# Optimization experiments

Measured on AMD Instinct MI355X. Metric: run time of the kernel, lower is better.

Reference implementation:

```python
import jax, jax.numpy as jnp
import numpy as np

B, IN_DIM, N, L = 8, 2, 512, 64
D_MODEL = 32
D_FF = 32          # must equal D_MODEL: output_bn is BatchNorm2d(d_model) applied to skip
DEPTH = 3          # blocks=3 * layers=1; dilation resets to 1 each block -> all dilations = 1
KS = 2             # temporal kernel size
EPS = 1e-5         # BatchNorm eps


def setup_inputs() -> dict:
    key = jax.random.key(0)
    ks = jax.random.split(key, 16)
    s = 0.1  # weight scale for numeric sanity
    x = jax.random.normal(ks[0], (B, IN_DIM, N, L), jnp.float32)
    a = jax.random.uniform(ks[1], (N, N), jnp.float32)
    adj = a / a.sum(axis=1, keepdims=True)  # row-stochastic diffusion matrix
    return {
        "x": x,
        "adj": adj,
        "Wstart": jax.random.normal(ks[2], (D_MODEL, IN_DIM), jnp.float32) * s,
        "bstart": jnp.zeros((D_MODEL,), jnp.float32),
        "Wf": jax.random.normal(ks[3], (DEPTH, D_MODEL, D_MODEL, KS), jnp.float32) * s,
        "bf": jnp.zeros((DEPTH, D_MODEL), jnp.float32),
        "Wg": jax.random.normal(ks[4], (DEPTH, D_MODEL, D_MODEL, KS), jnp.float32) * s,
        "bg": jnp.zeros((DEPTH, D_MODEL), jnp.float32),
        "Wskip": jax.random.normal(ks[5], (DEPTH, D_FF, D_MODEL), jnp.float32) * s,
        "bskip": jnp.zeros((DEPTH, D_FF), jnp.float32),
        "Wgc": jax.random.normal(ks[6], (DEPTH, D_MODEL, 3 * D_MODEL), jnp.float32) * s,
        "bgc": jnp.zeros((DEPTH, D_MODEL), jnp.float32),
        "gcbn_g": jnp.ones((DEPTH, D_MODEL), jnp.float32),
        "gcbn_b": jnp.zeros((DEPTH, D_MODEL), jnp.float32),
        "bn_g": jnp.ones((DEPTH, D_MODEL), jnp.float32),
        "bn_b": jnp.zeros((DEPTH, D_MODEL), jnp.float32),
        "obn_g": jnp.ones((D_MODEL,), jnp.float32),
        "obn_b": jnp.zeros((D_MODEL,), jnp.float32),
    }


def _c1x1(x, W, b):
    # Conv2d with (1,1) kernel == channel mixing. x: [b,c,n,l], W: [o,c]
    return jnp.einsum('bcnl,oc->bonl', x, W) + b[None, :, None, None]


def _dconv(x, W, b, d):
    # Conv2d kernel (1,2), dilation d along time (valid). W: [o,c,2]
    Lx = x.shape[-1]
    y = (jnp.einsum('bcnl,oc->bonl', x[..., :Lx - d], W[..., 0])
         + jnp.einsum('bcnl,oc->bonl', x[..., d:], W[..., 1]))
    return y + b[None, :, None, None]


def _bn(x, g, bta):
    # eval-mode BatchNorm2d: running_mean=0, running_var=1
    inv = g / jnp.sqrt(1.0 + EPS)
    return x * inv[None, :, None, None] + bta[None, :, None, None]


def reference(x, adj, Wstart, bstart, Wf, bf, Wg, bg, Wskip, bskip,
              Wgc, bgc, gcbn_g, gcbn_b, bn_g, bn_b, obn_g, obn_b):
    rf = 1 + DEPTH * (KS - 1)  # receptive field with dilation 1 per layer
    h = _c1x1(x, Wstart, bstart)
    if h.shape[-1] < rf:
        h = jnp.pad(h, ((0, 0), (0, 0), (0, 0), (rf - h.shape[-1], 0)))
    skip = None
    for i in range(DEPTH):
        residual = h
        filt = jnp.tanh(_dconv(h, Wf[i], bf[i], 1))
        gate = jax.nn.sigmoid(_dconv(h, Wg[i], bg[i], 1))
        h = filt * gate
        s = _c1x1(h, Wskip[i], bskip[i])
        skip = s if skip is None else s + skip[..., -s.shape[-1]:]
        if i == DEPTH - 1:
            break
        # order-2 graph diffusion: h, A h, A^2 h -> concat -> 1x1 conv -> BN (dropout: eval noop)
        x1 = jnp.einsum('bcnl,nm->bcml', h, adj)
        x2 = jnp.einsum('bcnl,nm->bcml', x1, adj)
        cat = jnp.concatenate([h, x1, x2], axis=1)
        g = _bn(_c1x1(cat, Wgc[i], bgc[i]), gcbn_g[i], gcbn_b[i])
        h = g + residual[..., -g.shape[-1]:]
        h = _bn(h, bn_g[i], bn_b[i])
    out = _bn(skip, obn_g, obn_b)
    return jnp.swapaxes(out, 1, 3)  # [B, L', N, C]
```

## Files before the change

### kernel.cpp

```cpp
#include <hip/hip_runtime.h>
#include <hip/hip_bf16.h>

#define B_     8
#define CIN_   2
#define N_     512
#define C_     32
#define L_     64
#define LOUT_  61
#define BUF_   ((size_t)(8*32*512*64))

typedef __hip_bfloat16 bf16;
typedef unsigned short ushort_t;
typedef unsigned int u32;
typedef __attribute__((ext_vector_type(8))) unsigned short us8;
typedef __attribute__((ext_vector_type(8))) short bf16x8;
typedef __attribute__((ext_vector_type(4))) float f32x4;

static __device__ __forceinline__ float bits2f(ushort_t u) {
    return __uint_as_float(((unsigned)u) << 16);
}
static __device__ __forceinline__ ushort_t f2bits(float v) {
    unsigned u = __float_as_uint(v);
    return (ushort_t)((u + 0x7fffu + ((u >> 16) & 1u)) >> 16);
}

static __device__ __forceinline__ void gload16(const ushort_t* g, ushort_t* l) {
    __builtin_amdgcn_global_load_lds(
        (const __attribute__((address_space(1))) unsigned int*)g,
        (__attribute__((address_space(3))) unsigned int*)l,
        16, 0, 0);
}

static __device__ __forceinline__ u32 swap1(u32 v) {
    return (u32)__builtin_amdgcn_update_dpp(0, (int)v, 0xB1, 0xF, 0xF, true);
}

__global__ void k_start(const float* __restrict__ x,
                        const float* __restrict__ Wst,
                        const float* __restrict__ bst,
                        ushort_t* __restrict__ h) {
    int idx = blockIdx.x * 256 + threadIdx.x;
    int l0 = (idx & 7) * 8;
    int n  = (idx >> 3) & 511;
    int o  = (idx >> 12) & 31;
    int b  = idx >> 17;
    float w0 = Wst[o * 2], w1 = Wst[o * 2 + 1], bb = bst[o];
    int xbase = (b * CIN_ * N_ + n) * L_ + l0;
    float va[8], vb[8];
    *(float4*)&va[0] = *(const float4*)(x + xbase);
    *(float4*)&va[4] = *(const float4*)(x + xbase + 4);
    *(float4*)&vb[0] = *(const float4*)(x + xbase + N_ * L_);
    *(float4*)&vb[4] = *(const float4*)(x + xbase + N_ * L_ + 4);
    us8 r;
    #pragma unroll
    for (int k = 0; k < 8; ++k) r[k] = f2bits(bb + va[k] * w0 + vb[k] * w1);
    *(us8*)(h + (size_t)idx * 8) = r;
}

__global__ void k_transA(const float* __restrict__ adj, ushort_t* __restrict__ adjT) {
    __shared__ float buf[64][65];
    int ti = blockIdx.x & 7;
    int tj = blockIdx.x >> 3;
    int t = threadIdx.x;
    for (int r = 0; r < 16; ++r) {
        int e = t + 256 * r;
        int rl = e >> 6, cl = e & 63;
        buf[rl][cl] = adj[(size_t)(ti * 64 + rl) * 512 + tj * 64 + cl];
    }
    __syncthreads();
    for (int r = 0; r < 16; ++r) {
        int e = t + 256 * r;
        int ml = e >> 6, nl = e & 63;
        adjT[(size_t)(tj * 64 + ml) * 512 + ti * 64 + nl] = f2bits(buf[nl][ml]);
    }
}

__global__ __launch_bounds__(256, 2) void k_sq(const ushort_t* __restrict__ adjT,
                                               ushort_t* __restrict__ adj2T) {
    __shared__ __align__(16) ushort_t lds2[8192];
    ushort_t* As = lds2;
    ushort_t* Bs = lds2 + 4096;
    int mt = blockIdx.x & 7, nc = blockIdx.x >> 3;
    int t = threadIdx.x, lane = t & 63, w = t >> 6;
    int la = lane & 15, q = lane >> 4;
    f32x4 acc[4];
    #pragma unroll
    for (int mi = 0; mi < 4; ++mi) acc[mi] = (f32x4)0.f;
    for (int p0 = 0; p0 < 512; p0 += 64) {
        __syncthreads();
        #pragma unroll
        for (int r = 0; r < 2; ++r) {
            int e = t + 256 * r, ml = e >> 3, oct = e & 7;
            int sw = ((oct + (ml >> 3)) & 7) << 3;
            *(us8*)(As + ml * 64 + sw) =
                *(const us8*)(adjT + (size_t)(mt * 64 + ml) * 512 + p0 + oct * 8);
            *(us8*)(Bs + ml * 64 + sw) =
                *(const us8*)(adjT + (size_t)(p0 + ml) * 512 + nc * 64 + oct * 8);
        }
        __syncthreads();
        #pragma unroll
        for (int ks = 0; ks < 2; ++ks) {
            bf16x8 a[4];
            #pragma unroll
            for (int mi = 0; mi < 4; ++mi) {
                int m = mi * 16 + la;
                int bl = (ks * 4 + q + (m >> 3)) & 7;
                a[mi] = *(const bf16x8*)(As + m * 64 + bl * 8);
            }
            bf16x8 bv;
            {
                int n = w * 16 + la;
                int rot = ((n >> 3) + ks * 4 + q) & 7;
                int col = rot * 8 + (n & 7);
                const ushort_t* p = Bs + (ks * 32 + q * 8) * 64 + col;
                #pragma unroll
                for (int j = 0; j < 8; ++j) bv[j] = (short)p[j * 64];
            }
            #pragma unroll
            for (int mi = 0; mi < 4; ++mi)
                acc[mi] = __builtin_amdgcn_mfma_f32_16x16x32_bf16(a[mi], bv, acc[mi], 0, 0, 0);
        }
    }
    __syncthreads();
    ushort_t* Ys = lds2;
    #pragma unroll
    for (int mi = 0; mi < 4; ++mi)
        #pragma unroll
        for (int r = 0; r < 4; ++r)
            Ys[(mi * 16 + q * 4 + r) * 72 + w * 16 + la] = f2bits(acc[mi][r]);
    __syncthreads();
    #pragma unroll
    for (int r = 0; r < 2; ++r) {
        int e = t + 256 * r, ml = e >> 3, oct = e & 7;
        us8 v = *(const us8*)(Ys + ml * 72 + oct * 8);
        *(us8*)(adj2T + (size_t)(mt * 64 + ml) * 512 + nc * 64 + oct * 8) = v;
    }
}

__global__ __launch_bounds__(256, 4) void k_gs_mfma(
        const ushort_t* __restrict__ h,
        const float* __restrict__ Wf, const float* __restrict__ bfp,
        const float* __restrict__ Wg, const float* __restrict__ bgp,
        const float* __restrict__ Wsk, const float* __restrict__ bsk,
        ushort_t* __restrict__ G, float* __restrict__ out,
        int off, int mode, int storeG,
        const float* __restrict__ og, const float* __restrict__ obb) {
    __shared__ __align__(16) ushort_t lds[9984];
    ushort_t* Hs  = lds;
    ushort_t* Asf = lds + 4096;
    ushort_t* Asg = lds + 6400;
    ushort_t* As2 = lds + 8704;
    __shared__ float bfv[32], bgv[32], bsv[32];
    int t = threadIdx.x;
    int b = blockIdx.x >> 8, n0 = (blockIdx.x & 255) * 2;
    int lane = t & 63, w = t >> 6;
    int ng = w & 1, cg = w >> 1;
    int la = lane & 15, q = lane >> 4;

    const ushort_t* hb = h + (size_t)(b * 32) * 512 * 64;
    #pragma unroll
    for (int r = 0; r < 2; ++r) {
        int e = t + 256 * r;
        int row = e >> 3, s = e & 7;
        int og_ = ((s - row - (row >> 5)) & 7) * 8;
        gload16(hb + ((size_t)(row >> 1) * 512 + n0 + (row & 1)) * 64 + og_,
                Hs + (size_t)e * 8);
    }
    {
        int o = t >> 3, k8 = (t & 7) * 8;
        us8 vf, vg;
        #pragma unroll
        for (int i = 0; i < 8; ++i) {
            int k = k8 + i, c = k & 31, tap = k >> 5;
            vf[i] = f2bits(Wf[o * 64 + c * 2 + tap]);
            vg[i] = f2bits(Wg[o * 64 + c * 2 + tap]);
        }
        *(us8*)(Asf + o * 72 + k8) = vf;
        *(us8*)(Asg + o * 72 + k8) = vg;
        if (k8 < 32) {
            us8 vs;
            #pragma unroll
            for (int i = 0; i < 8; ++i) vs[i] = f2bits(Wsk[o * 32 + k8 + i]);
            *(us8*)(As2 + o * 40 + k8) = vs;
        }
        if (t < 32) { bfv[t] = bfp[t]; bgv[t] = bgp[t]; bsv[t] = bsk[t]; }
    }
    float4 oldv[4];
    #pragma unroll
    for (int i = 0; i < 4; ++i) oldv[i] = make_float4(0.f, 0.f, 0.f, 0.f);
    {
        int col = t >> 1, o0 = (t & 1) * 16;
        int nr = col >> 6, l = col & 63;
        if (mode != 0 && l < LOUT_) {
            const float* po = out + ((size_t)(b * LOUT_ + l) * 512 + n0 + nr) * 32 + o0;
            #pragma unroll
            for (int i = 0; i < 4; ++i) oldv[i] = *(const float4*)(po + i * 4);
        }
    }
    __syncthreads();

    bf16x8 af[2][2], ag[2][2];
    #pragma unroll
    for (int mt = 0; mt < 2; ++mt)
        #pragma unroll
        for (int ks = 0; ks < 2; ++ks) {
            af[mt][ks] = *(const bf16x8*)(Asf + (mt * 16 + la) * 72 + ks * 32 + q * 8);
            ag[mt][ks] = *(const bf16x8*)(Asg + (mt * 16 + la) * 72 + ks * 32 + q * 8);
        }
    bf16x8 a2[2];
    a2[0] = *(const bf16x8*)(As2 + la * 40 + q * 8);
    a2[1] = *(const bf16x8*)(As2 + (16 + la) * 40 + q * 8);

    f32x4 fa[2][2], ga[2][2];
    #pragma unroll
    for (int mt = 0; mt < 2; ++mt)
        #pragma unroll
        for (int cl = 0; cl < 2; ++cl) { fa[mt][cl] = (f32x4)0.f; ga[mt][cl] = (f32x4)0.f; }
    #pragma unroll
    for (int cl = 0; cl < 2; ++cl) {
        int ct = cg * 2 + cl;
        #pragma unroll
        for (int ks = 0; ks < 2; ++ks) {
            int le = ct * 16 + la + ks;
            bf16x8 bv;
            #pragma unroll
            for (int j = 0; j < 8; ++j) {
                int row = (q * 8 + j) * 2 + ng;
                int slot = ((le >> 3) + row + (row >> 5)) & 7;
                bv[j] = (le < 64) ? (short)Hs[row * 64 + (slot & 7) * 8 + (le & 7)] : (short)0;
            }
            #pragma unroll
            for (int mt = 0; mt < 2; ++mt) {
                fa[mt][cl] = __builtin_amdgcn_mfma_f32_16x16x32_bf16(af[mt][ks], bv, fa[mt][cl], 0, 0, 0);
                ga[mt][cl] = __builtin_amdgcn_mfma_f32_16x16x32_bf16(ag[mt][ks], bv, ga[mt][cl], 0, 0, 0);
            }
        }
    }
    __syncthreads();

    #pragma unroll
    for (int mt = 0; mt < 2; ++mt)
        #pragma unroll
        for (int cl = 0; cl < 2; ++cl)
            #pragma unroll
            for (int r = 0; r < 4; ++r) {
                int o = mt * 16 + q * 4 + r;
                float fv = fa[mt][cl][r] + bfv[o];
                float gv = ga[mt][cl][r] + bgv[o];
                float ef = __expf(2.f * fv);
                float act = (1.f - 2.f / (ef + 1.f)) * (1.f / (1.f + __expf(-gv)));
                int l = (cg * 2 + cl) * 16 + la;
                int row = o * 2 + ng;
                int slot = ((l >> 3) + row + (row >> 5)) & 7;
                Hs[row * 64 + slot * 8 + (l & 7)] = f2bits(act);
            }
    __syncthreads();

    if (storeG) {
        #pragma unroll
        for (int r = 0; r < 2; ++r) {
            int e = t + 256 * r;
            int row = e >> 3, s = e & 7;
            int og_ = (s - row - (row >> 5)) & 7;
            us8 v = *(const us8*)(Hs + (size_t)e * 8);
            *(us8*)(G + ((size_t)(b * 32 + (row >> 1)) * 512 + n0 + (row & 1)) * 64 + og_ * 8) = v;
        }
    }
    f32x4 sa[2][2];
    #pragma unroll
    for (int mt = 0; mt < 2; ++mt)
        #pragma unroll
        for (int cl = 0; cl < 2; ++cl) sa[mt][cl] = (f32x4)0.f;
    #pragma unroll
    for (int cl = 0; cl < 2; ++cl) {
        int le = (cg * 2 + cl) * 16 + la + off;
        bf16x8 bv;
        #pragma unroll
        for (int j = 0; j < 8; ++j) {
            int row = (q * 8 + j) * 2 + ng;
            int slot = ((le >> 3) + row + (row >> 5)) & 7;
            bv[j] = (le < 64) ? (short)Hs[row * 64 + (slot & 7) * 8 + (le & 7)] : (short)0;
        }
        sa[0][cl] = __builtin_amdgcn_mfma_f32_16x16x32_bf16(a2[0], bv, sa[0][cl], 0, 0, 0);
        sa[1][cl] = __builtin_amdgcn_mfma_f32_16x16x32_bf16(a2[1], bv, sa[1][cl], 0, 0, 0);
    }
    __syncthreads();

    float* St = (float*)lds;
    const float rbn = rsqrtf(1.f + 1e-5f);
    #pragma unroll
    for (int mt = 0; mt < 2; ++mt)
        #pragma unroll
        for (int cl = 0; cl < 2; ++cl) {
            int col = ng * 64 + (cg * 2 + cl) * 16 + la;
            int ob = mt * 16 + q * 4;
            float4 sv = make_float4(sa[mt][cl][0] + bsv[ob],
                                    sa[mt][cl][1] + bsv[ob + 1],
                                    sa[mt][cl][2] + bsv[ob + 2],
                                    sa[mt][cl][3] + bsv[ob + 3]);
            *(float4*)(St + col * 36 + ob) = sv;
        }
    __syncthreads();
    {
        int col = t >> 1, o0 = (t & 1) * 16;
        int nr = col >> 6, l = col & 63;
        if (l < LOUT_) {
            float* po = out + ((size_t)(b * LOUT_ + l) * 512 + n0 + nr) * 32 + o0;
            #pragma unroll
            for (int i = 0; i < 4; ++i) {
                float4 s = *(float4*)(St + col * 36 + o0 + i * 4);
                if (mode == 0) {
                    *(float4*)(po + i * 4) = s;
                } else {
                    float4 vv = make_float4(oldv[i].x + s.x, oldv[i].y + s.y,
                                            oldv[i].z + s.z, oldv[i].w + s.w);
                    if (mode == 2) {
                        int ob = o0 + i * 4;
                        vv.x = vv.x * (og[ob] * rbn) + obb[ob];
                        vv.y = vv.y * (og[ob + 1] * rbn) + obb[ob + 1];
                        vv.z = vv.z * (og[ob + 2] * rbn) + obb[ob + 2];
                        vv.w = vv.w * (og[ob + 3] * rbn) + obb[ob + 3];
                    }
                    *(float4*)(po + i * 4) = vv;
                }
            }
        }
    }
}

__global__ __launch_bounds__(256, 4) void k_diffuse2(
        const ushort_t* __restrict__ X, const ushort_t* __restrict__ adjT,
        const ushort_t* __restrict__ adj2T,
        ushort_t* __restrict__ Y1, ushort_t* __restrict__ Y2) {
    __shared__ __align__(16) ushort_t lds[16384];
    int cp = blockIdx.x & 15;
    int mt = (blockIdx.x >> 4) & 7;
    int b  = blockIdx.x >> 7;
    int t  = threadIdx.x;
    int lane = t & 63, w = t >> 6;
    int c_loc = w & 1, lh = w >> 1;
    int m0 = mt * 64;
    int la = lane & 15, q = lane >> 4;
    int p_ = la & 1;
    u32 sel = p_ ? 0x07060302u : 0x05040100u;
    const ushort_t* Xb = X + (size_t)(b * 32 + cp * 2) * 512 * 64;
    f32x4 acc1[4][2], acc2[4][2];
    #pragma unroll
    for (int mi = 0; mi < 4; ++mi)
        #pragma unroll
        for (int li = 0; li < 2; ++li) { acc1[mi][li] = (f32x4)0.f; acc2[mi][li] = (f32x4)0.f; }

    union U { u32 u[4]; bf16x8 v; };

    auto STAGE = [&](int n0, ushort_t* bb) {
        ushort_t* As1b = bb;
        ushort_t* As2b = bb + 2048;
        ushort_t* Xsb  = bb + 4096;
        {
            int ml = t >> 2, g = t & 3;
            gload16(adjT  + (size_t)(m0 + ml) * 512 + n0 + g * 8, As1b + (size_t)t * 8);
            gload16(adj2T + (size_t)(m0 + ml) * 512 + n0 + g * 8, As2b + (size_t)t * 8);
        }
        #pragma unroll
        for (int r = 0; r < 2; ++r) {
            int e = t + 256 * r;
            int cl = e >> 8, nl = (e >> 3) & 31, s = e & 7;
            int og = ((s - nl - (nl >> 3)) & 7) * 8;
            gload16(Xb + ((size_t)cl * 512 + n0 + nl) * 64 + og, Xsb + (size_t)e * 8);
        }
    };

    STAGE(0, lds);
    __syncthreads();

    for (int it = 0; it < 16; ++it) {
        ushort_t* cur = lds + (it & 1) * 8192;
        if (it < 15) STAGE((it + 1) * 32, lds + ((it + 1) & 1) * 8192);
        ushort_t* As1 = cur;
        ushort_t* As2 = cur + 2048;
        ushort_t* Xs  = cur + 4096;
        const ushort_t* xc = Xs + c_loc * 2048;
        bf16x8 a1[4], a2v[4];
        #pragma unroll
        for (int mi = 0; mi < 4; ++mi) {
            int m = mi * 16 + la;
            a1[mi]  = *(const bf16x8*)(As1 + m * 32 + q * 8);
            a2v[mi] = *(const bf16x8*)(As2 + m * 32 + q * 8);
        }
        bf16x8 bb[2];
        #pragma unroll
        for (int li = 0; li < 2; ++li) {
            int l2 = lh * 32 + li * 16 + (la & ~1);
            int r0 = q * 8 + p_ * 4;
            int brot = ((l2 >> 3) + p_ * 4 + q) & 7;
            u32 o0 = *(const u32*)(xc + (r0 + 0) * 64 + (((brot + 0) & 7) << 3) + (l2 & 7));
            u32 o1 = *(const u32*)(xc + (r0 + 1) * 64 + (((brot + 1) & 7) << 3) + (l2 & 7));
            u32 o2 = *(const u32*)(xc + (r0 + 2) * 64 + (((brot + 2) & 7) << 3) + (l2 & 7));
            u32 o3 = *(const u32*)(xc + (r0 + 3) * 64 + (((brot + 3) & 7) << 3) + (l2 & 7));
            u32 s0 = swap1(o0), s1 = swap1(o1), s2 = swap1(o2), s3 = swap1(o3);
            u32 lo0 = p_ ? s0 : o0, lo1 = p_ ? s1 : o1;
            u32 lo2 = p_ ? s2 : o2, lo3 = p_ ? s3 : o3;
            u32 hi0 = p_ ? o0 : s0, hi1 = p_ ? o1 : s1;
            u32 hi2 = p_ ? o2 : s2, hi3 = p_ ? o3 : s3;
            U u;
            u.u[0] = __builtin_amdgcn_perm(lo1, lo0, sel);
            u.u[1] = __builtin_amdgcn_perm(lo3, lo2, sel);
            u.u[2] = __builtin_amdgcn_perm(hi1, hi0, sel);
            u.u[3] = __builtin_amdgcn_perm(hi3, hi2, sel);
            bb[li] = u.v;
        }
        #pragma unroll
        for (int mi = 0; mi < 4; ++mi)
            #pragma unroll
            for (int li = 0; li < 2; ++li) {
                acc1[mi][li] = __builtin_amdgcn_mfma_f32_16x16x32_bf16(a1[mi],  bb[li], acc1[mi][li], 0, 0, 0);
                acc2[mi][li] = __builtin_amdgcn_mfma_f32_16x16x32_bf16(a2v[mi], bb[li], acc2[mi][li], 0, 0, 0);
            }
        __syncthreads();
    }

    ushort_t* Ys = lds;
    #pragma unroll
    for (int pass = 0; pass < 2; ++pass) {
        __syncthreads();
        f32x4 (*src)[2] = pass ? acc2 : acc1;
        #pragma unroll
        for (int mi = 0; mi < 4; ++mi)
            #pragma unroll
            for (int li = 0; li < 2; ++li)
                #pragma unroll
                for (int r = 0; r < 4; ++r) {
                    int row = mi * 16 + q * 4 + r;
                    int col = lh * 32 + li * 16 + la;
                    Ys[c_loc * 4608 + row * 72 + col] = f2bits(src[mi][li][r]);
                }
        __syncthreads();
        ushort_t* Yo = pass ? Y2 : Y1;
        int c = t >> 7, mrem = t & 127;
        int m = mrem >> 1, lq = mrem & 1;
        #pragma unroll
        for (int r = 0; r < 4; ++r) {
            int l0 = lq * 32 + r * 8;
            us8 v = *(const us8*)(Ys + c * 4608 + m * 72 + l0);
            *(us8*)(Yo + ((size_t)(b * 32 + cp * 2 + c) * 512 + m0 + m) * 64 + l0) = v;
        }
    }
}

__global__ __launch_bounds__(256, 4) void k_gc3_mfma(
        ushort_t* __restrict__ G, const ushort_t* __restrict__ X1,
        const ushort_t* __restrict__ X2, const ushort_t* __restrict__ hres,
        const float* __restrict__ Wgc, const float* __restrict__ bgc,
        const float* __restrict__ gg, const float* __restrict__ gb,
        const float* __restrict__ bg2, const float* __restrict__ bb2) {
    __shared__ __align__(16) ushort_t cat[192 * 64];
    __shared__ __align__(16) ushort_t hr[64 * 64];
    __shared__ __align__(16) ushort_t Aw[32 * 104];
    __shared__ float prm[5][32];
    int t = threadIdx.x;
    int b = blockIdx.x >> 8, n0 = (blockIdx.x & 255) * 2;
    int lane = t & 63, w = t >> 6;
    int ng = w & 1, cg = w >> 1;
    int la = lane & 15, q = lane >> 4;
    int p_ = la & 1;
    u32 sel = p_ ? 0x07060302u : 0x05040100u;

    #pragma unroll
    for (int r = 0; r < 6; ++r) {
        int e = t + 256 * r;
        int row = e >> 3, s = e & 7;
        int k = row >> 1, nr = row & 1;
        int rot = k + (k >> 3);
        int og = ((s - rot) & 7) * 8;
        const ushort_t* src = (k < 32) ? G : ((k < 64) ? X1 : X2);
        gload16(src + ((size_t)(b * 32 + (k & 31)) * 512 + n0 + nr) * 64 + og,
                cat + (size_t)e * 8);
    }
    #pragma unroll
    for (int r = 0; r < 2; ++r) {
        int e = t + 256 * r;
        int row = e >> 3, oct = e & 7;
        gload16(hres + ((size_t)(b * 32 + (row >> 1)) * 512 + n0 + (row & 1)) * 64 + oct * 8,
                hr + (size_t)e * 8);
    }
    for (int e = t; e < 384; e += 256) {
        int o = e / 12, oct = e % 12;
        us8 v;
        #pragma unroll
        for (int i = 0; i < 8; ++i) v[i] = f2bits(Wgc[o * 96 + oct * 8 + i]);
        *(us8*)(Aw + o * 104 + oct * 8) = v;
    }
    if (t < 32) {
        prm[0][t] = bgc[t]; prm[1][t] = gg[t]; prm[2][t] = gb[t];
        prm[3][t] = bg2[t]; prm[4][t] = bb2[t];
    }
    __syncthreads();

    bf16x8 a[2][3];
    #pragma unroll
    for (int mt = 0; mt < 2; ++mt)
        #pragma unroll
        for (int ks = 0; ks < 3; ++ks)
            a[mt][ks] = *(const bf16x8*)(Aw + (mt * 16 + la) * 104 + ks * 32 + q * 8);

    union U { u32 u[4]; bf16x8 v; };
    f32x4 acc[2][2];
    #pragma unroll
    for (int mt = 0; mt < 2; ++mt)
        #pragma unroll
        for (int cl = 0; cl < 2; ++cl) acc[mt][cl] = (f32x4)0.f;
    #pragma unroll
    for (int cl = 0; cl < 2; ++cl) {
        int l2 = (cg * 2 + cl) * 16 + (la & ~1);
        #pragma unroll
        for (int ks = 0; ks < 3; ++ks) {
            int rb = (ks * 64 + q * 16 + p_ * 8 + ng);
            int brot = ((l2 >> 3) + p_ * 4 + ks * 4 + q) & 7;
            u32 o0 = *(const u32*)(cat + (rb + 0) * 64 + (((brot + 0) & 7) << 3) + (l2 & 7));
            u32 o1 = *(const u32*)(cat + (rb + 2) * 64 + (((brot + 1) & 7) << 3) + (l2 & 7));
            u32 o2 = *(const u32*)(cat + (rb + 4) * 64 + (((brot + 2) & 7) << 3) + (l2 & 7));
            u32 o3 = *(const u32*)(cat + (rb + 6) * 64 + (((brot + 3) & 7) << 3) + (l2 & 7));
            u32 s0 = swap1(o0), s1 = swap1(o1), s2 = swap1(o2), s3 = swap1(o3);
            u32 lo0 = p_ ? s0 : o0, lo1 = p_ ? s1 : o1;
            u32 lo2 = p_ ? s2 : o2, lo3 = p_ ? s3 : o3;
            u32 hi0 = p_ ? o0 : s0, hi1 = p_ ? o1 : s1;
            u32 hi2 = p_ ? o2 : s2, hi3 = p_ ? o3 : s3;
            U u;
            u.u[0] = __builtin_amdgcn_perm(lo1, lo0, sel);
            u.u[1] = __builtin_amdgcn_perm(lo3, lo2, sel);
            u.u[2] = __builtin_amdgcn_perm(hi1, hi0, sel);
            u.u[3] = __builtin_amdgcn_perm(hi3, hi2, sel);
            acc[0][cl] = __builtin_amdgcn_mfma_f32_16x16x32_bf16(a[0][ks], u.v, acc[0][cl], 0, 0, 0);
            acc[1][cl] = __builtin_amdgcn_mfma_f32_16x16x32_bf16(a[1][ks], u.v, acc[1][cl], 0, 0, 0);
        }
    }
    __syncthreads();

    const float rbn = rsqrtf(1.f + 1e-5f);
    #pragma unroll
    for (int mt = 0; mt < 2; ++mt)
        #pragma unroll
        for (int cl = 0; cl < 2; ++cl)
            #pragma unroll
            for (int r = 0; r < 4; ++r) {
                int o = mt * 16 + q * 4 + r;
                int l = (cg * 2 + cl) * 16 + la;
                float v = acc[mt][cl][r] + prm[0][o];
                v = v * (prm[1][o] * rbn) + prm[2][o];
                float res = (l < 63) ? bits2f(hr[(o * 2 + ng) * 64 + l + 1]) : 0.f;
                v = (v + res) * (prm[3][o] * rbn) + prm[4][o];
                int row = o * 2 + ng;
                int rot = o + (o >> 3);
                int slot = ((l >> 3) + rot) & 7;
                cat[row * 64 + slot * 8 + (l & 7)] = f2bits(v);
            }
    __syncthreads();
    #pragma unroll
    for (int r = 0; r < 2; ++r) {
        int e = t + 256 * r;
        int row = e >> 3, og = e & 7;
        int o = row >> 1, nr = row & 1;
        int slot = (og + o + (o >> 3)) & 7;
        us8 v = *(const us8*)(cat + row * 64 + slot * 8);
        *(us8*)(G + ((size_t)(b * 32 + o) * 512 + n0 + nr) * 64 + og * 8) = v;
    }
}

extern "C" void kernel_launch(void* const* d_in, const int* in_sizes, int n_in,
                              void* d_out, int out_size, void* d_ws, size_t ws_size,
                              hipStream_t stream) {
    const float* x      = (const float*)d_in[0];
    const float* adj    = (const float*)d_in[1];
    const float* Wstart = (const float*)d_in[2];
    const float* bstart = (const float*)d_in[3];
    const float* Wf     = (const float*)d_in[4];
    const float* bf_    = (const float*)d_in[5];
    const float* Wg     = (const float*)d_in[6];
    const float* bg     = (const float*)d_in[7];
    const float* Wskip  = (const float*)d_in[8];
    const float* bskip  = (const float*)d_in[9];
    const float* Wgc    = (const float*)d_in[10];
    const float* bgc    = (const float*)d_in[11];
    const float* gcbn_g = (const float*)d_in[12];
    const float* gcbn_b = (const float*)d_in[13];
    const float* bn_g   = (const float*)d_in[14];
    const float* bn_b   = (const float*)d_in[15];
    const float* obn_g  = (const float*)d_in[16];
    const float* obn_b  = (const float*)d_in[17];
    float* out = (float*)d_out;

    ushort_t* P0    = (ushort_t*)d_ws;
    ushort_t* P1    = P0 + BUF_;
    ushort_t* P2    = P1 + BUF_;
    ushort_t* P3    = P2 + BUF_;
    ushort_t* adjT  = P3 + BUF_;
    ushort_t* adj2T = adjT + 512 * 512;

    k_transA<<<64, 256, 0, stream>>>(adj, adjT);
    k_sq<<<64, 256, 0, stream>>>(adjT, adj2T);
    k_start<<<4096, 256, 0, stream>>>(x, Wstart, bstart, P0);

    ushort_t* h  = P0;
    ushort_t* Gb = P1;
    for (int i = 0; i < 3; ++i) {
        int mode = (i == 0) ? 0 : ((i == 2) ? 2 : 1);
        k_gs_mfma<<<2048, 256, 0, stream>>>(h, Wf + i * 2048, bf_ + i * 32,
                                            Wg + i * 2048, bg + i * 32,
                                            Wskip + i * 1024, bskip + i * 32,
                                            Gb, out, 2 - i, mode, (i < 2) ? 1 : 0,
                                            obn_g, obn_b);
        if (i == 2) break;
        k_diffuse2<<<1024, 256, 0, stream>>>(Gb, adjT, adj2T, P2, P3);
        k_gc3_mfma<<<2048, 256, 0, stream>>>(Gb, P2, P3, h,
                                             Wgc + i * 3072, bgc + i * 32,
                                             gcbn_g + i * 32, gcbn_b + i * 32,
                                             bn_g + i * 32, bn_b + i * 32);
        ushort_t* tmp = h; h = Gb; Gb = tmp;
    }
}
```

Baseline: 295.6 us.

## Apply graph-conv channel mixing before diffusion and fuse diffusion with GC epilogue

Uses linearity to move the 1x1 graph-conv weight ahead of the adjacency diffusion: the gated-activation kernel now computes three projected maps (W0·h, W1·h, W2·h) and writes them out. A combined diffusion kernel then multiplies by A and A² and applies bias, both batchnorms and the residual in its epilogue, which removes the separate gc3 kernel and the round trip of the diffusion outputs. The diffusion kernel now stages two B operands, which doubles its LDS use and lowers occupancy to 3 blocks. The gs kernel also does extra MFMAs and writes three buffers instead of one.

```diff
diff --git a/kernel.cpp b/kernel.cpp
--- a/kernel.cpp
+++ b/kernel.cpp
@@ -142,14 +142,18 @@
         const float* __restrict__ Wf, const float* __restrict__ bfp,
         const float* __restrict__ Wg, const float* __restrict__ bgp,
         const float* __restrict__ Wsk, const float* __restrict__ bsk,
-        ushort_t* __restrict__ G, float* __restrict__ out,
-        int off, int mode, int storeG,
+        const float* __restrict__ Wgc,
+        ushort_t* __restrict__ H0, ushort_t* __restrict__ H1, ushort_t* __restrict__ H2,
+        float* __restrict__ out,
+        int off, int mode, int doH,
         const float* __restrict__ og, const float* __restrict__ obb) {
-    __shared__ __align__(16) ushort_t lds[9984];
+    __shared__ __align__(16) ushort_t lds[13824];
     ushort_t* Hs  = lds;
     ushort_t* Asf = lds + 4096;
     ushort_t* Asg = lds + 6400;
     ushort_t* As2 = lds + 8704;
+    ushort_t* AwH = lds + 9984;
+    ushort_t* Hst = lds + 4096;
     __shared__ float bfv[32], bgv[32], bsv[32];
     int t = threadIdx.x;
     int b = blockIdx.x >> 8, n0 = (blockIdx.x & 255) * 2;
@@ -184,6 +188,15 @@
             *(us8*)(As2 + o * 40 + k8) = vs;
         }
         if (t < 32) { bfv[t] = bfp[t]; bgv[t] = bgp[t]; bsv[t] = bsk[t]; }
+    }
+    if (doH) {
+        for (int e = t; e < 384; e += 256) {
+            int j = e >> 7, rem = e & 127, o = rem >> 2, g = rem & 3;
+            us8 v;
+            #pragma unroll
+            for (int i = 0; i < 8; ++i) v[i] = f2bits(Wgc[o * 96 + j * 32 + g * 8 + i]);
+            *(us8*)(AwH + j * 1280 + o * 40 + g * 8) = v;
+        }
     }
     float4 oldv[4];
     #pragma unroll
@@ -256,16 +269,6 @@
             }
     __syncthreads();
 
-    if (storeG) {
-        #pragma unroll
-        for (int r = 0; r < 2; ++r) {
-            int e = t + 256 * r;
-            int row = e >> 3, s = e & 7;
-            int og_ = (s - row - (row >> 5)) & 7;
-            us8 v = *(const us8*)(Hs + (size_t)e * 8);
-            *(us8*)(G + ((size_t)(b * 32 + (row >> 1)) * 512 + n0 + (row & 1)) * 64 + og_ * 8) = v;
-        }
-    }
     f32x4 sa[2][2];
     #pragma unroll
     for (int mt = 0; mt < 2; ++mt)
@@ -283,6 +286,56 @@
         }
         sa[0][cl] = __builtin_amdgcn_mfma_f32_16x16x32_bf16(a2[0], bv, sa[0][cl], 0, 0, 0);
         sa[1][cl] = __builtin_amdgcn_mfma_f32_16x16x32_bf16(a2[1], bv, sa[1][cl], 0, 0, 0);
+    }
+
+    if (doH) {
+        bf16x8 bv0[2];
+        #pragma unroll
+        for (int cl = 0; cl < 2; ++cl) {
+            int le = (cg * 2 + cl) * 16 + la;
+            #pragma unroll
+            for (int j = 0; j < 8; ++j) {
+                int row = (q * 8 + j) * 2 + ng;
+                int slot = ((le >> 3) + row + (row >> 5)) & 7;
+                bv0[cl][j] = (short)Hs[row * 64 + slot * 8 + (le & 7)];
+            }
+        }
+        ushort_t* dsts[3] = {H0, H1, H2};
+        #pragma unroll
+        for (int j = 0; j < 3; ++j) {
+            bf16x8 aH0 = *(const bf16x8*)(AwH + j * 1280 + la * 40 + q * 8);
+            bf16x8 aH1 = *(const bf16x8*)(AwH + j * 1280 + (16 + la) * 40 + q * 8);
+            f32x4 sh[2][2];
+            #pragma unroll
+            for (int mt = 0; mt < 2; ++mt)
+                #pragma unroll
+                for (int cl = 0; cl < 2; ++cl) sh[mt][cl] = (f32x4)0.f;
+            #pragma unroll
+            for (int cl = 0; cl < 2; ++cl) {
+                sh[0][cl] = __builtin_amdgcn_mfma_f32_16x16x32_bf16(aH0, bv0[cl], sh[0][cl], 0, 0, 0);
+                sh[1][cl] = __builtin_amdgcn_mfma_f32_16x16x32_bf16(aH1, bv0[cl], sh[1][cl], 0, 0, 0);
+            }
+            #pragma unroll
+            for (int mt = 0; mt < 2; ++mt)
+                #pragma unroll
+                for (int cl = 0; cl < 2; ++cl)
+                    #pragma unroll
+                    for (int r = 0; r < 4; ++r) {
+                        int o = mt * 16 + q * 4 + r;
+                        int l = (cg * 2 + cl) * 16 + la;
+                        Hst[(o * 2 + ng) * 72 + l] = f2bits(sh[mt][cl][r]);
+                    }
+            __syncthreads();
+            ushort_t* dst = dsts[j];
+            #pragma unroll
+            for (int r = 0; r < 2; ++r) {
+                int e = t + 256 * r;
+                int row = e >> 3, oct = e & 7;
+                us8 v = *(const us8*)(Hst + row * 72 + oct * 8);
+                *(us8*)(dst + ((size_t)(b * 32 + (row >> 1)) * 512 + n0 + (row & 1)) * 64 + oct * 8) = v;
+            }
+            __syncthreads();
+        }
     }
     __syncthreads();
 
@@ -328,11 +381,15 @@
     }
 }
 
-__global__ __launch_bounds__(256, 4) void k_diffuse2(
-        const ushort_t* __restrict__ X, const ushort_t* __restrict__ adjT,
-        const ushort_t* __restrict__ adj2T,
-        ushort_t* __restrict__ Y1, ushort_t* __restrict__ Y2) {
-    __shared__ __align__(16) ushort_t lds[16384];
+__global__ __launch_bounds__(256, 3) void k_diffgc(
+        ushort_t* __restrict__ H0, const ushort_t* __restrict__ H1,
+        const ushort_t* __restrict__ H2, const ushort_t* __restrict__ hres,
+        const ushort_t* __restrict__ adjT, const ushort_t* __restrict__ adj2T,
+        const float* __restrict__ bgc, const float* __restrict__ gg,
+        const float* __restrict__ gb, const float* __restrict__ bg2,
+        const float* __restrict__ bb2) {
+    __shared__ __align__(16) ushort_t lds[24576];
+    __shared__ float prm[5][32];
     int cp = blockIdx.x & 15;
     int mt = (blockIdx.x >> 4) & 7;
     int b  = blockIdx.x >> 7;
@@ -343,7 +400,12 @@
     int la = lane & 15, q = lane >> 4;
     int p_ = la & 1;
     u32 sel = p_ ? 0x07060302u : 0x05040100u;
-    const ushort_t* Xb = X + (size_t)(b * 32 + cp * 2) * 512 * 64;
+    const ushort_t* B1b = H1 + (size_t)(b * 32 + cp * 2) * 512 * 64;
+    const ushort_t* B2b = H2 + (size_t)(b * 32 + cp * 2) * 512 * 64;
+    if (t < 32) {
+        prm[0][t] = bgc[t]; prm[1][t] = gg[t]; prm[2][t] = gb[t];
+        prm[3][t] = bg2[t]; prm[4][t] = bb2[t];
+    }
     f32x4 acc1[4][2], acc2[4][2];
     #pragma unroll
     for (int mi = 0; mi < 4; ++mi)
@@ -355,7 +417,8 @@
     auto STAGE = [&](int n0, ushort_t* bb) {
         ushort_t* As1b = bb;
         ushort_t* As2b = bb + 2048;
-        ushort_t* Xsb  = bb + 4096;
+        ushort_t* B1sb = bb + 4096;
+        ushort_t* B2sb = bb + 8192;
         {
             int ml = t >> 2, g = t & 3;
             gload16(adjT  + (size_t)(m0 + ml) * 512 + n0 + g * 8, As1b + (size_t)t * 8);
@@ -366,7 +429,8 @@
             int e = t + 256 * r;
             int cl = e >> 8, nl = (e >> 3) & 31, s = e & 7;
             int og = ((s - nl - (nl >> 3)) & 7) * 8;
-            gload16(Xb + ((size_t)cl * 512 + n0 + nl) * 64 + og, Xsb + (size_t)e * 8);
+            gload16(B1b + ((size_t)cl * 512 + n0 + nl) * 64 + og, B1sb + (size_t)e * 8);
+            gload16(B2b + ((size_t)cl * 512 + n0 + nl) * 64 + og, B2sb + (size_t)e * 8);
         }
     };
 
@@ -374,12 +438,12 @@
     __syncthreads();
 
     for (int it = 0; it < 16; ++it) {
-        ushort_t* cur = lds + (it & 1) * 8192;
-        if (it < 15) STAGE((it + 1) * 32, lds + ((it + 1) & 1) * 8192);
+        ushort_t* cur = lds + (it & 1) * 12288;
+        if (it < 15) STAGE((it + 1) * 32, lds + ((it + 1) & 1) * 12288);
         ushort_t* As1 = cur;
         ushort_t* As2 = cur + 2048;
-        ushort_t* Xs  = cur + 4096;
-        const ushort_t* xc = Xs + c_loc * 2048;
+        const ushort_t* xc1 = cur + 4096 + c_loc * 2048;
+        const ushort_t* xc2 = cur + 8192 + c_loc * 2048;
         bf16x8 a1[4], a2v[4];
         #pragma unroll
         for (int mi = 0; mi < 4; ++mi) {
@@ -387,182 +451,95 @@
             a1[mi]  = *(const bf16x8*)(As1 + m * 32 + q * 8);
             a2v[mi] = *(const bf16x8*)(As2 + m * 32 + q * 8);
         }
-        bf16x8 bb[2];
+        bf16x8 bb1[2], bb2[2];
         #pragma unroll
         for (int li = 0; li < 2; ++li) {
             int l2 = lh * 32 + li * 16 + (la & ~1);
             int r0 = q * 8 + p_ * 4;
             int brot = ((l2 >> 3) + p_ * 4 + q) & 7;
-            u32 o0 = *(const u32*)(xc + (r0 + 0) * 64 + (((brot + 0) & 7) << 3) + (l2 & 7));
-            u32 o1 = *(const u32*)(xc + (r0 + 1) * 64 + (((brot + 1) & 7) << 3) + (l2 & 7));
-            u32 o2 = *(const u32*)(xc + (r0 + 2) * 64 + (((brot + 2) & 7) << 3) + (l2 & 7));
-            u32 o3 = *(const u32*)(xc + (r0 + 3) * 64 + (((brot + 3) & 7) << 3) + (l2 & 7));
-            u32 s0 = swap1(o0), s1 = swap1(o1), s2 = swap1(o2), s3 = swap1(o3);
-            u32 lo0 = p_ ? s0 : o0, lo1 = p_ ? s1 : o1;
-            u32 lo2 = p_ ? s2 : o2, lo3 = p_ ? s3 : o3;
-            u32 hi0 = p_ ? o0 : s0, hi1 = p_ ? o1 : s1;
-            u32 hi2 = p_ ? o2 : s2, hi3 = p_ ? o3 : s3;
-            U u;
-            u.u[0] = __builtin_amdgcn_perm(lo1, lo0, sel);
-            u.u[1] = __builtin_amdgcn_perm(lo3, lo2, sel);
-            u.u[2] = __builtin_amdgcn_perm(hi1, hi0, sel);
-            u.u[3] = __builtin_amdgcn_perm(hi3, hi2, sel);
-            bb[li] = u.v;
+            #pragma unroll
+            for (int src = 0; src < 2; ++src) {
+                const ushort_t* xc = src ? xc2 : xc1;
+                u32 o0 = *(const u32*)(xc + (r0 + 0) * 64 + (((brot + 0) & 7) << 3) + (l2 & 7));
+                u32 o1 = *(const u32*)(xc + (r0 + 1) * 64 + (((brot + 1) & 7) << 3) + (l2 & 7));
+                u32 o2 = *(const u32*)(xc + (r0 + 2) * 64 + (((brot + 2) & 7) << 3) + (l2 & 7));
+                u32 o3 = *(const u32*)(xc + (r0 + 3) * 64 + (((brot + 3) & 7) << 3) + (l2 & 7));
+                u32 s0 = swap1(o0), s1 = swap1(o1), s2 = swap1(o2), s3 = swap1(o3);
+                u32 lo0 = p_ ? s0 : o0, lo1 = p_ ? s1 : o1;
+                u32 lo2 = p_ ? s2 : o2, lo3 = p_ ? s3 : o3;
+                u32 hi0 = p_ ? o0 : s0, hi1 = p_ ? o1 : s1;
+                u32 hi2 = p_ ? o2 : s2, hi3 = p_ ? o3 : s3;
+                U u;
+                u.u[0] = __builtin_amdgcn_perm(lo1, lo0, sel);
+                u.u[1] = __builtin_amdgcn_perm(lo3, lo2, sel);
+                u.u[2] = __builtin_amdgcn_perm(hi1, hi0, sel);
+                u.u[3] = __builtin_amdgcn_perm(hi3, hi2, sel);
+                if (src) bb2[li] = u.v; else bb1[li] = u.v;
+            }
         }
         #pragma unroll
         for (int mi = 0; mi < 4; ++mi)
             #pragma unroll
             for (int li = 0; li < 2; ++li) {
-                acc1[mi][li] = __builtin_amdgcn_mfma_f32_16x16x32_bf16(a1[mi],  bb[li], acc1[mi][li], 0, 0, 0);
-                acc2[mi][li] = __builtin_amdgcn_mfma_f32_16x16x32_bf16(a2v[mi], bb[li], acc2[mi][li], 0, 0, 0);
+                acc1[mi][li] = __builtin_amdgcn_mfma_f32_16x16x32_bf16(a1[mi],  bb1[li], acc1[mi][li], 0, 0, 0);
+                acc2[mi][li] = __builtin_amdgcn_mfma_f32_16x16x32_bf16(a2v[mi], bb2[li], acc2[mi][li], 0, 0, 0);
             }
         __syncthreads();
     }
 
+    ushort_t* H0s = lds;
+    ushort_t* HRs = lds + 8192;
+    #pragma unroll
+    for (int r = 0; r < 4; ++r) {
+        int e = t + 256 * r;
+        int ch = e >> 9, m = (e >> 3) & 63, g = e & 7;
+        gload16(H0   + ((size_t)(b * 32 + cp * 2 + ch) * 512 + m0 + m) * 64 + g * 8,
+                H0s + (size_t)e * 8);
+        gload16(hres + ((size_t)(b * 32 + cp * 2 + ch) * 512 + m0 + m) * 64 + g * 8,
+                HRs + (size_t)e * 8);
+    }
+    __syncthreads();
+
+    const float rbn = rsqrtf(1.f + 1e-5f);
+    int op = cp * 2 + c_loc;
+    #pragma unroll
+    for (int mi = 0; mi < 4; ++mi)
+        #pragma unroll
+        for (int li = 0; li < 2; ++li)
+            #pragma unroll
+            for (int r = 0; r < 4; ++r) {
+                int row = mi * 16 + q * 4 + r;
+                int col = lh * 32 + li * 16 + la;
+                float v = acc1[mi][li][r] + acc2[mi][li][r]
+                        + bits2f(H0s[c_loc * 4096 + row * 64 + col]) + prm[0][op];
+                v = v * (prm[1][op] * rbn) + prm[2][op];
+                float res = (col < 63) ? bits2f(HRs[c_loc * 4096 + row * 64 + col + 1]) : 0.f;
+                v = (v + res) * (prm[3][op] * rbn) + prm[4][op];
+                acc1[mi][li][r] = v;
+            }
+    __syncthreads();
+
     ushort_t* Ys = lds;
     #pragma unroll
-    for (int pass = 0; pass < 2; ++pass) {
-        __syncthreads();
-        f32x4 (*src)[2] = pass ? acc2 : acc1;
-        #pragma unroll
-        for (int mi = 0; mi < 4; ++mi)
-            #pragma unroll
-            for (int li = 0; li < 2; ++li)
-                #pragma unroll
-                for (int r = 0; r < 4; ++r) {
-                    int row = mi * 16 + q * 4 + r;
-                    int col = lh * 32 + li * 16 + la;
-                    Ys[c_loc * 4608 + row * 72 + col] = f2bits(src[mi][li][r]);
-                }
-        __syncthreads();
-        ushort_t* Yo = pass ? Y2 : Y1;
+    for (int mi = 0; mi < 4; ++mi)
+        #pragma unroll
+        for (int li = 0; li < 2; ++li)
+            #pragma unroll
+            for (int r = 0; r < 4; ++r) {
+                int row = mi * 16 + q * 4 + r;
+                int col = lh * 32 + li * 16 + la;
+                Ys[c_loc * 4608 + row * 72 + col] = f2bits(acc1[mi][li][r]);
+            }
+    __syncthreads();
+    {
         int c = t >> 7, mrem = t & 127;
         int m = mrem >> 1, lq = mrem & 1;
         #pragma unroll
         for (int r = 0; r < 4; ++r) {
             int l0 = lq * 32 + r * 8;
             us8 v = *(const us8*)(Ys + c * 4608 + m * 72 + l0);
-            *(us8*)(Yo + ((size_t)(b * 32 + cp * 2 + c) * 512 + m0 + m) * 64 + l0) = v;
-        }
-    }
-}
-
-__global__ __launch_bounds__(256, 4) void k_gc3_mfma(
-        ushort_t* __restrict__ G, const ushort_t* __restrict__ X1,
-        const ushort_t* __restrict__ X2, const ushort_t* __restrict__ hres,
-        const float* __restrict__ Wgc, const float* __restrict__ bgc,
-        const float* __restrict__ gg, const float* __restrict__ gb,
-        const float* __restrict__ bg2, const float* __restrict__ bb2) {
-    __shared__ __align__(16) ushort_t cat[192 * 64];
-    __shared__ __align__(16) ushort_t hr[64 * 64];
-    __shared__ __align__(16) ushort_t Aw[32 * 104];
-    __shared__ float prm[5][32];
-    int t = threadIdx.x;
-    int b = blockIdx.x >> 8, n0 = (blockIdx.x & 255) * 2;
-    int lane = t & 63, w = t >> 6;
-    int ng = w & 1, cg = w >> 1;
-    int la = lane & 15, q = lane >> 4;
-    int p_ = la & 1;
-    u32 sel = p_ ? 0x07060302u : 0x05040100u;
-
-    #pragma unroll
-    for (int r = 0; r < 6; ++r) {
-        int e = t + 256 * r;
-        int row = e >> 3, s = e & 7;
-        int k = row >> 1, nr = row & 1;
-        int rot = k + (k >> 3);
-        int og = ((s - rot) & 7) * 8;
-        const ushort_t* src = (k < 32) ? G : ((k < 64) ? X1 : X2);
-        gload16(src + ((size_t)(b * 32 + (k & 31)) * 512 + n0 + nr) * 64 + og,
-                cat + (size_t)e * 8);
-    }
-    #pragma unroll
-    for (int r = 0; r < 2; ++r) {
-        int e = t + 256 * r;
-        int row = e >> 3, oct = e & 7;
-        gload16(hres + ((size_t)(b * 32 + (row >> 1)) * 512 + n0 + (row & 1)) * 64 + oct * 8,
-                hr + (size_t)e * 8);
-    }
-    for (int e = t; e < 384; e += 256) {
-        int o = e / 12, oct = e % 12;
-        us8 v;
-        #pragma unroll
-        for (int i = 0; i < 8; ++i) v[i] = f2bits(Wgc[o * 96 + oct * 8 + i]);
-        *(us8*)(Aw + o * 104 + oct * 8) = v;
-    }
-    if (t < 32) {
-        prm[0][t] = bgc[t]; prm[1][t] = gg[t]; prm[2][t] = gb[t];
-        prm[3][t] = bg2[t]; prm[4][t] = bb2[t];
-    }
-    __syncthreads();
-
-    bf16x8 a[2][3];
-    #pragma unroll
-    for (int mt = 0; mt < 2; ++mt)
-        #pragma unroll
-        for (int ks = 0; ks < 3; ++ks)
-            a[mt][ks] = *(const bf16x8*)(Aw + (mt * 16 + la) * 104 + ks * 32 + q * 8);
-
-    union U { u32 u[4]; bf16x8 v; };
-    f32x4 acc[2][2];
-    #pragma unroll
-    for (int mt = 0; mt < 2; ++mt)
-        #pragma unroll
-        for (int cl = 0; cl < 2; ++cl) acc[mt][cl] = (f32x4)0.f;
-    #pragma unroll
-    for (int cl = 0; cl < 2; ++cl) {
-        int l2 = (cg * 2 + cl) * 16 + (la & ~1);
-        #pragma unroll
-        for (int ks = 0; ks < 3; ++ks) {
-            int rb = (ks * 64 + q * 16 + p_ * 8 + ng);
-            int brot = ((l2 >> 3) + p_ * 4 + ks * 4 + q) & 7;
-            u32 o0 = *(const u32*)(cat + (rb + 0) * 64 + (((brot + 0) & 7) << 3) + (l2 & 7));
-            u32 o1 = *(const u32*)(cat + (rb + 2) * 64 + (((brot + 1) & 7) << 3) + (l2 & 7));
-            u32 o2 = *(const u32*)(cat + (rb + 4) * 64 + (((brot + 2) & 7) << 3) + (l2 & 7));
-            u32 o3 = *(const u32*)(cat + (rb + 6) * 64 + (((brot + 3) & 7) << 3) + (l2 & 7));
-            u32 s0 = swap1(o0), s1 = swap1(o1), s2 = swap1(o2), s3 = swap1(o3);
-            u32 lo0 = p_ ? s0 : o0, lo1 = p_ ? s1 : o1;
-            u32 lo2 = p_ ? s2 : o2, lo3 = p_ ? s3 : o3;
-            u32 hi0 = p_ ? o0 : s0, hi1 = p_ ? o1 : s1;
-            u32 hi2 = p_ ? o2 : s2, hi3 = p_ ? o3 : s3;
-            U u;
-            u.u[0] = __builtin_amdgcn_perm(lo1, lo0, sel);
-            u.u[1] = __builtin_amdgcn_perm(lo3, lo2, sel);
-            u.u[2] = __builtin_amdgcn_perm(hi1, hi0, sel);
-            u.u[3] = __builtin_amdgcn_perm(hi3, hi2, sel);
-            acc[0][cl] = __builtin_amdgcn_mfma_f32_16x16x32_bf16(a[0][ks], u.v, acc[0][cl], 0, 0, 0);
-            acc[1][cl] = __builtin_amdgcn_mfma_f32_16x16x32_bf16(a[1][ks], u.v, acc[1][cl], 0, 0, 0);
-        }
-    }
-    __syncthreads();
-
-    const float rbn = rsqrtf(1.f + 1e-5f);
-    #pragma unroll
-    for (int mt = 0; mt < 2; ++mt)
-        #pragma unroll
-        for (int cl = 0; cl < 2; ++cl)
-            #pragma unroll
-            for (int r = 0; r < 4; ++r) {
-                int o = mt * 16 + q * 4 + r;
-                int l = (cg * 2 + cl) * 16 + la;
-                float v = acc[mt][cl][r] + prm[0][o];
-                v = v * (prm[1][o] * rbn) + prm[2][o];
-                float res = (l < 63) ? bits2f(hr[(o * 2 + ng) * 64 + l + 1]) : 0.f;
-                v = (v + res) * (prm[3][o] * rbn) + prm[4][o];
-                int row = o * 2 + ng;
-                int rot = o + (o >> 3);
-                int slot = ((l >> 3) + rot) & 7;
-                cat[row * 64 + slot * 8 + (l & 7)] = f2bits(v);
-            }
-    __syncthreads();
-    #pragma unroll
-    for (int r = 0; r < 2; ++r) {
-        int e = t + 256 * r;
-        int row = e >> 3, og = e & 7;
-        int o = row >> 1, nr = row & 1;
-        int slot = (og + o + (o >> 3)) & 7;
-        us8 v = *(const us8*)(cat + row * 64 + slot * 8);
-        *(us8*)(G + ((size_t)(b * 32 + o) * 512 + n0 + nr) * 64 + og * 8) = v;
+            *(us8*)(H0 + ((size_t)(b * 32 + cp * 2 + c) * 512 + m0 + m) * 64 + l0) = v;
+        }
     }
 }
 
@@ -600,21 +577,20 @@
     k_sq<<<64, 256, 0, stream>>>(adjT, adj2T);
     k_start<<<4096, 256, 0, stream>>>(x, Wstart, bstart, P0);
 
-    ushort_t* h  = P0;
-    ushort_t* Gb = P1;
+    ushort_t* h   = P0;
+    ushort_t* alt = P1;
     for (int i = 0; i < 3; ++i) {
         int mode = (i == 0) ? 0 : ((i == 2) ? 2 : 1);
         k_gs_mfma<<<2048, 256, 0, stream>>>(h, Wf + i * 2048, bf_ + i * 32,
                                             Wg + i * 2048, bg + i * 32,
                                             Wskip + i * 1024, bskip + i * 32,
-                                            Gb, out, 2 - i, mode, (i < 2) ? 1 : 0,
+                                            Wgc + i * 3072,
+                                            alt, P2, P3, out, 2 - i, mode, (i < 2) ? 1 : 0,
                                             obn_g, obn_b);
         if (i == 2) break;
-        k_diffuse2<<<1024, 256, 0, stream>>>(Gb, adjT, adj2T, P2, P3);
-        k_gc3_mfma<<<2048, 256, 0, stream>>>(Gb, P2, P3, h,
-                                             Wgc + i * 3072, bgc + i * 32,
-                                             gcbn_g + i * 32, gcbn_b + i * 32,
-                                             bn_g + i * 32, bn_b + i * 32);
-        ushort_t* tmp = h; h = Gb; Gb = tmp;
-    }
-}
+        k_diffgc<<<1024, 256, 0, stream>>>(alt, P2, P3, h, adjT, adj2T,
+                                           bgc + i * 32, gcbn_g + i * 32, gcbn_b + i * 32,
+                                           bn_g + i * 32, bn_b + i * 32);
+        ushort_t* nh = alt; alt = h; h = nh;
+    }
+}
```

Measured after the change: 295.9 us. No clear change (+0.1%).
